# Optimization experiments

Measured on AMD Instinct MI355X. Metric: run time of the kernel, lower is better.

The kernel has to match this reference:

```python
import jax, jax.numpy as jnp
import numpy as np


def setup_inputs() -> dict:
    key = jax.random.key(0)
    k_u, k_a, k_b, k_c, k_d = jax.random.split(key, 5)
    B, T, Din, Dout, S = 16, 4096, 256, 256, 256
    return {
        "u": jax.random.normal(k_u, (B, T, Din), dtype=jnp.float32),
        "a_raw": jnp.zeros((S,), dtype=jnp.float32),
        "b": jax.random.normal(k_b, (S, Din), dtype=jnp.float32) * 0.1,
        "c": jax.random.normal(k_c, (Dout, S), dtype=jnp.float32) * 0.1,
        "d": jax.random.normal(k_d, (Dout, Din), dtype=jnp.float32) * 0.1,
    }


def reference(u, a_raw, b, c, d):
    # u: (B, T, Din) -> y: (B, T, Dout)
    # Recurrence: x_t = a * x_{t-1} + b @ u_t ;  y_t = c @ x_t + d @ u_t
    a = jnp.tanh(a_raw)                                  # (S,)
    Bu = jnp.einsum('btd,sd->bts', u, b)                 # input projection, (B,T,S)

    def step(x, bu_t):
        x = x * a + bu_t                                 # diagonal state update
        return x, x

    x0 = jnp.zeros((u.shape[0], a.shape[0]), dtype=u.dtype)
    _, xs = jax.lax.scan(step, x0, jnp.swapaxes(Bu, 0, 1))  # xs: (T,B,S)
    xs = jnp.swapaxes(xs, 0, 1)                              # (B,T,S)

    y = jnp.einsum('bts,os->bto', xs, c) + jnp.einsum('bti,oi->bto', u, d)
    return y  # dropout(p=0.0) is identity
```

## Files before the change

kernel.cpp:

```cpp
#include <hip/hip_runtime.h>

#define DEV __device__ __forceinline__

typedef unsigned short u16;
typedef __attribute__((ext_vector_type(8))) __bf16 bf16x8;
typedef __attribute__((ext_vector_type(4))) float f32x4;
typedef __attribute__((ext_vector_type(8))) unsigned short u16x8;

static constexpr int NB = 16;
static constexpr int NT = 4096;
static constexpr int ND = 256;
static constexpr int NM = NB * NT;
static constexpr int NCH = 64;
static constexpr int LCH = 64;

DEV u16 f2bf(float f) {
  unsigned u = __builtin_bit_cast(unsigned, f);
  u += 0x7fffu + ((u >> 16) & 1u);
  return (u16)(u >> 16);
}
DEV float bf2f(u16 h) {
  unsigned u = ((unsigned)h) << 16;
  return __builtin_bit_cast(float, u);
}

DEV void gl_lds16(const void* gp, void* lp) {
  __builtin_amdgcn_global_load_lds(
      (__attribute__((address_space(1))) void*)(void*)gp,
      (__attribute__((address_space(3))) void*)lp, 16, 0, 0);
}

__global__ __launch_bounds__(256) void prep_k(const float* __restrict__ a_raw,
                                              const float* __restrict__ b,
                                              const float* __restrict__ c,
                                              const float* __restrict__ d,
                                              float* __restrict__ af,
                                              u16* __restrict__ bw,
                                              u16* __restrict__ cw,
                                              u16* __restrict__ dw) {
  int i = blockIdx.x * 256 + threadIdx.x;
  if (i < 256) af[i] = tanhf(a_raw[i]);
  bw[i] = f2bf(b[i]);
  cw[i] = f2bf(c[i]);
  dw[i] = f2bf(d[i]);
}

__global__ __launch_bounds__(256) void convu_k(const float* __restrict__ u,
                                               u16* __restrict__ ub) {
  size_t i = ((size_t)blockIdx.x * 256 + threadIdx.x) * 8;
  float4 v0 = *reinterpret_cast<const float4*>(u + i);
  float4 v1 = *reinterpret_cast<const float4*>(u + i + 4);
  u16x8 o;
  o[0] = f2bf(v0.x); o[1] = f2bf(v0.y); o[2] = f2bf(v0.z); o[3] = f2bf(v0.w);
  o[4] = f2bf(v1.x); o[5] = f2bf(v1.y); o[6] = f2bf(v1.z); o[7] = f2bf(v1.w);
  *reinterpret_cast<u16x8*>(ub + i) = o;
}

template <int NSRC, bool OUT_BF16>
__global__ __launch_bounds__(256) void gemm_k(const u16* __restrict__ A0,
                                              const u16* __restrict__ B0,
                                              const u16* __restrict__ A1,
                                              const u16* __restrict__ B1,
                                              void* __restrict__ out) {
  __shared__ u16 As[128 * 64];
  __shared__ u16 Bs[128 * 64];
  const int tid = threadIdx.x;
  const int lane = tid & 63;
  const int wid = tid >> 6;
  const int wm = wid >> 1, wn = wid & 1;
  const int row0 = blockIdx.x * 128;
  const int col0 = blockIdx.y * 128;

  const int rstg = tid >> 3;
  const int c16 = tid & 7;

  const f32x4 zero = {0.f, 0.f, 0.f, 0.f};
  f32x4 acc[4][4];
#pragma unroll
  for (int i = 0; i < 4; ++i)
#pragma unroll
    for (int j = 0; j < 4; ++j) acc[i][j] = zero;

#pragma unroll
  for (int kt = 0; kt < 4 * NSRC; ++kt) {
    const u16* Ap = (NSRC == 2 && kt >= 4) ? A1 : A0;
    const u16* Bp = (NSRC == 2 && kt >= 4) ? B1 : B0;
    const int kb = (kt & 3) * 64;
#pragma unroll
    for (int j = 0; j < 4; ++j) {
      int row = j * 32 + rstg;
      int sc = c16 ^ (row & 7);
      gl_lds16(Ap + (size_t)(row0 + row) * 256 + kb + sc * 8,
               (char*)As + j * 4096 + wid * 1024);
      gl_lds16(Bp + (size_t)(col0 + row) * 256 + kb + sc * 8,
               (char*)Bs + j * 4096 + wid * 1024);
    }
    __syncthreads();
#pragma unroll
    for (int kk = 0; kk < 2; ++kk) {
      bf16x8 af[4], bfr[4];
#pragma unroll
      for (int mi = 0; mi < 4; ++mi) {
        int row = wm * 64 + mi * 16 + (lane & 15);
        int slot = (kk * 4 + (lane >> 4)) ^ (row & 7);
        af[mi] = *reinterpret_cast<const bf16x8*>(&As[row * 64 + slot * 8]);
      }
#pragma unroll
      for (int ni = 0; ni < 4; ++ni) {
        int row = wn * 64 + ni * 16 + (lane & 15);
        int slot = (kk * 4 + (lane >> 4)) ^ (row & 7);
        bfr[ni] = *reinterpret_cast<const bf16x8*>(&Bs[row * 64 + slot * 8]);
      }
#pragma unroll
      for (int mi = 0; mi < 4; ++mi)
#pragma unroll
        for (int ni = 0; ni < 4; ++ni)
          acc[mi][ni] = __builtin_amdgcn_mfma_f32_16x16x32_bf16(
              af[mi], bfr[ni], acc[mi][ni], 0, 0, 0);
    }
    __syncthreads();
  }

#pragma unroll
  for (int mi = 0; mi < 4; ++mi) {
    int rowb = row0 + wm * 64 + mi * 16 + (lane >> 4) * 4;
#pragma unroll
    for (int ni = 0; ni < 4; ++ni) {
      int colg = col0 + wn * 64 + ni * 16 + (lane & 15);
      f32x4 v = acc[mi][ni];
#pragma unroll
      for (int r = 0; r < 4; ++r) {
        size_t idx = (size_t)(rowb + r) * 256 + colg;
        if constexpr (OUT_BF16)
          ((u16*)out)[idx] = f2bf(v[r]);
        else
          ((float*)out)[idx] = v[r];
      }
    }
  }
}

__global__ __launch_bounds__(256) void scan1_k(const u16* __restrict__ bu,
                                               const float* __restrict__ af,
                                               float* __restrict__ carry) {
  int blk = blockIdx.x;
  int b = blk >> 6, ch = blk & 63;
  int s = threadIdx.x;
  float a = af[s];
  size_t base = ((size_t)(b * NT + ch * LCH)) * 256 + s;
  float x = 0.f;
  for (int tb = 0; tb < LCH; tb += 8) {
    float vb[8];
#pragma unroll
    for (int j = 0; j < 8; ++j) vb[j] = bf2f(bu[base + (size_t)(tb + j) * 256]);
#pragma unroll
    for (int j = 0; j < 8; ++j) x = fmaf(a, x, vb[j]);
  }
  carry[(size_t)blk * 256 + s] = x;
}

__global__ __launch_bounds__(256) void scan2_k(const float* __restrict__ carry,
                                               const float* __restrict__ af,
                                               float* __restrict__ initb) {
  int b = blockIdx.x;
  int s = threadIdx.x;
  float a = af[s];
  float aL = a;
#pragma unroll
  for (int i = 0; i < 6; ++i) aL *= aL;
  float x = 0.f;
  for (int k = 0; k < NCH; ++k) {
    size_t idx = ((size_t)(b * NCH + k)) * 256 + s;
    float cv = carry[idx];
    initb[idx] = x;
    x = fmaf(aL, x, cv);
  }
}

__global__ __launch_bounds__(256) void scan3_k(u16* __restrict__ bu,
                                               const float* __restrict__ af,
                                               const float* __restrict__ initb) {
  int blk = blockIdx.x;
  int b = blk >> 6, ch = blk & 63;
  int s = threadIdx.x;
  float a = af[s];
  float x = initb[(size_t)blk * 256 + s];
  size_t base = ((size_t)(b * NT + ch * LCH)) * 256 + s;
  for (int tb = 0; tb < LCH; tb += 8) {
    float vb[8];
#pragma unroll
    for (int j = 0; j < 8; ++j) vb[j] = bf2f(bu[base + (size_t)(tb + j) * 256]);
    u16 ob[8];
#pragma unroll
    for (int j = 0; j < 8; ++j) {
      x = fmaf(a, x, vb[j]);
      ob[j] = f2bf(x);
    }
#pragma unroll
    for (int j = 0; j < 8; ++j) bu[base + (size_t)(tb + j) * 256] = ob[j];
  }
}

extern "C" void kernel_launch(void* const* d_in, const int* in_sizes, int n_in,
                              void* d_out, int out_size, void* d_ws, size_t ws_size,
                              hipStream_t stream) {
  const float* u = (const float*)d_in[0];
  const float* a_raw = (const float*)d_in[1];
  const float* b = (const float*)d_in[2];
  const float* c = (const float*)d_in[3];
  const float* d = (const float*)d_in[4];
  float* y = (float*)d_out;
  char* ws = (char*)d_ws;

  float* af = (float*)(ws);
  u16* bw = (u16*)(ws + 4096);
  u16* cw = (u16*)(ws + 4096 + 131072);
  u16* dw = (u16*)(ws + 4096 + 2 * 131072);
  u16* ubf = (u16*)(ws + (1 << 20));
  u16* bu = (u16*)(ws + (1 << 20) + (size_t)32 * 1024 * 1024);
  float* carry = (float*)(ws + (1 << 20) + (size_t)64 * 1024 * 1024);
  float* initb = (float*)(ws + (2 << 20) + (size_t)64 * 1024 * 1024);

  prep_k<<<256, 256, 0, stream>>>(a_raw, b, c, d, af, bw, cw, dw);
  convu_k<<<8192, 256, 0, stream>>>(u, ubf);
  gemm_k<1, true><<<dim3(512, 2), 256, 0, stream>>>(ubf, bw, nullptr, nullptr, bu);
  scan1_k<<<1024, 256, 0, stream>>>(bu, af, carry);
  scan2_k<<<16, 256, 0, stream>>>(carry, af, initb);
  scan3_k<<<1024, 256, 0, stream>>>(bu, af, initb);
  gemm_k<2, false><<<dim3(512, 2), 256, 0, stream>>>(bu, cw, ubf, dw, y);
}
```

Measured before the change: 96.79 us.

## Fuse fp32 conversion into first GEMM and scan pass into second GEMM

Drops the separate u-to-bf16 conversion kernel by converting fp32 u inside the first GEMM. That GEMM now also computes the D·u product, which the second GEMM uses as its accumulator initial value. The third scan pass moves into the second GEMM: each block loads a 128-row bu tile into LDS, runs the chunk recurrence in place, then multiplies by C. It also stores bu in a swizzled layout so it can be bulk-copied to LDS, and widens the scan1 loads. This removes several full-tensor round trips through HBM. The cost is a larger LDS footprint (about 80KB per block), which limits occupancy, plus a serial 64-step scan inside the GEMM before the MFMA work starts.

```diff
diff --git a/kernel.cpp b/kernel.cpp
--- a/kernel.cpp
+++ b/kernel.cpp
@@ -6,11 +6,10 @@
 typedef __attribute__((ext_vector_type(8))) __bf16 bf16x8;
 typedef __attribute__((ext_vector_type(4))) float f32x4;
 typedef __attribute__((ext_vector_type(8))) unsigned short u16x8;
+typedef __attribute__((ext_vector_type(4))) unsigned short u16x4;
 
 static constexpr int NB = 16;
 static constexpr int NT = 4096;
-static constexpr int ND = 256;
-static constexpr int NM = NB * NT;
 static constexpr int NCH = 64;
 static constexpr int LCH = 64;
 
@@ -28,6 +27,13 @@
   __builtin_amdgcn_global_load_lds(
       (__attribute__((address_space(1))) void*)(void*)gp,
       (__attribute__((address_space(3))) void*)lp, 16, 0, 0);
+}
+
+DEV u16x8 pack8(float4 a, float4 b) {
+  u16x8 o;
+  o[0] = f2bf(a.x); o[1] = f2bf(a.y); o[2] = f2bf(a.z); o[3] = f2bf(a.w);
+  o[4] = f2bf(b.x); o[5] = f2bf(b.y); o[6] = f2bf(b.z); o[7] = f2bf(b.w);
+  return o;
 }
 
 __global__ __launch_bounds__(256) void prep_k(const float* __restrict__ a_raw,
@@ -45,96 +51,89 @@
   dw[i] = f2bf(d[i]);
 }
 
-__global__ __launch_bounds__(256) void convu_k(const float* __restrict__ u,
-                                               u16* __restrict__ ub) {
-  size_t i = ((size_t)blockIdx.x * 256 + threadIdx.x) * 8;
-  float4 v0 = *reinterpret_cast<const float4*>(u + i);
-  float4 v1 = *reinterpret_cast<const float4*>(u + i + 4);
-  u16x8 o;
-  o[0] = f2bf(v0.x); o[1] = f2bf(v0.y); o[2] = f2bf(v0.z); o[3] = f2bf(v0.w);
-  o[4] = f2bf(v1.x); o[5] = f2bf(v1.y); o[6] = f2bf(v1.z); o[7] = f2bf(v1.w);
-  *reinterpret_cast<u16x8*>(ub + i) = o;
-}
-
-template <int NSRC, bool OUT_BF16>
-__global__ __launch_bounds__(256) void gemm_k(const u16* __restrict__ A0,
-                                              const u16* __restrict__ B0,
-                                              const u16* __restrict__ A1,
-                                              const u16* __restrict__ B1,
-                                              void* __restrict__ out) {
+__global__ __launch_bounds__(512) void gemm1_k(const float* __restrict__ u,
+                                               const u16* __restrict__ bw,
+                                               const u16* __restrict__ dw,
+                                               u16* __restrict__ bu,
+                                               u16* __restrict__ ud) {
   __shared__ u16 As[128 * 64];
   __shared__ u16 Bs[128 * 64];
   const int tid = threadIdx.x;
   const int lane = tid & 63;
   const int wid = tid >> 6;
-  const int wm = wid >> 1, wn = wid & 1;
-  const int row0 = blockIdx.x * 128;
-  const int col0 = blockIdx.y * 128;
-
-  const int rstg = tid >> 3;
-  const int c16 = tid & 7;
+  const int wr = wid >> 2, wc = wid & 3;
+  const int bx = blockIdx.x;
+  const int by = blockIdx.y;
+  const bool dpanel = (by >= 2);
+  const int col0 = (by & 1) * 128;
+  const u16* W = dpanel ? dw : bw;
+  const size_t row0 = (size_t)bx * 128;
+
+  const int arow = tid >> 2;
+  const int ak0 = (tid & 3) * 16;
+  const float* uptr = u + (row0 + arow) * 256;
+  const int s0 = (tid & 3) * 2;
 
   const f32x4 zero = {0.f, 0.f, 0.f, 0.f};
-  f32x4 acc[4][4];
-#pragma unroll
-  for (int i = 0; i < 4; ++i)
-#pragma unroll
-    for (int j = 0; j < 4; ++j) acc[i][j] = zero;
-
-#pragma unroll
-  for (int kt = 0; kt < 4 * NSRC; ++kt) {
-    const u16* Ap = (NSRC == 2 && kt >= 4) ? A1 : A0;
-    const u16* Bp = (NSRC == 2 && kt >= 4) ? B1 : B0;
-    const int kb = (kt & 3) * 64;
-#pragma unroll
-    for (int j = 0; j < 4; ++j) {
-      int row = j * 32 + rstg;
-      int sc = c16 ^ (row & 7);
-      gl_lds16(Ap + (size_t)(row0 + row) * 256 + kb + sc * 8,
-               (char*)As + j * 4096 + wid * 1024);
-      gl_lds16(Bp + (size_t)(col0 + row) * 256 + kb + sc * 8,
-               (char*)Bs + j * 4096 + wid * 1024);
-    }
+  f32x4 acc[4][2];
+#pragma unroll
+  for (int i = 0; i < 4; ++i) { acc[i][0] = zero; acc[i][1] = zero; }
+
+#pragma unroll
+  for (int kt = 0; kt < 4; ++kt) {
+    const int kb = kt * 64;
+    float4 f0 = *reinterpret_cast<const float4*>(uptr + kb + ak0);
+    float4 f1 = *reinterpret_cast<const float4*>(uptr + kb + ak0 + 4);
+    float4 f2 = *reinterpret_cast<const float4*>(uptr + kb + ak0 + 8);
+    float4 f3 = *reinterpret_cast<const float4*>(uptr + kb + ak0 + 12);
+#pragma unroll
+    for (int r = 0; r < 2; ++r) {
+      int brow = r * 64 + (tid >> 3);
+      int sc = (tid & 7) ^ (brow & 7);
+      gl_lds16(W + (size_t)(col0 + brow) * 256 + kb + sc * 8,
+               (char*)Bs + r * 8192 + wid * 1024);
+    }
+    *reinterpret_cast<u16x8*>(&As[arow * 64 + ((s0) ^ (arow & 7)) * 8]) = pack8(f0, f1);
+    *reinterpret_cast<u16x8*>(&As[arow * 64 + ((s0 + 1) ^ (arow & 7)) * 8]) = pack8(f2, f3);
     __syncthreads();
 #pragma unroll
     for (int kk = 0; kk < 2; ++kk) {
-      bf16x8 af[4], bfr[4];
+      const int ks = kk * 4 + (lane >> 4);
+      bf16x8 afr[4], bfr[2];
 #pragma unroll
       for (int mi = 0; mi < 4; ++mi) {
-        int row = wm * 64 + mi * 16 + (lane & 15);
-        int slot = (kk * 4 + (lane >> 4)) ^ (row & 7);
-        af[mi] = *reinterpret_cast<const bf16x8*>(&As[row * 64 + slot * 8]);
-      }
-#pragma unroll
-      for (int ni = 0; ni < 4; ++ni) {
-        int row = wn * 64 + ni * 16 + (lane & 15);
-        int slot = (kk * 4 + (lane >> 4)) ^ (row & 7);
-        bfr[ni] = *reinterpret_cast<const bf16x8*>(&Bs[row * 64 + slot * 8]);
+        int ar = wr * 64 + mi * 16 + (lane & 15);
+        afr[mi] = *reinterpret_cast<const bf16x8*>(&As[ar * 64 + (ks ^ (ar & 7)) * 8]);
+      }
+#pragma unroll
+      for (int ni = 0; ni < 2; ++ni) {
+        int nr = wc * 32 + ni * 16 + (lane & 15);
+        bfr[ni] = *reinterpret_cast<const bf16x8*>(&Bs[nr * 64 + (ks ^ (nr & 7)) * 8]);
       }
 #pragma unroll
       for (int mi = 0; mi < 4; ++mi)
 #pragma unroll
-        for (int ni = 0; ni < 4; ++ni)
+        for (int ni = 0; ni < 2; ++ni)
           acc[mi][ni] = __builtin_amdgcn_mfma_f32_16x16x32_bf16(
-              af[mi], bfr[ni], acc[mi][ni], 0, 0, 0);
-    }
-    __syncthreads();
+              afr[mi], bfr[ni], acc[mi][ni], 0, 0, 0);
+    }
+    if (kt < 3) __syncthreads();
   }
 
 #pragma unroll
   for (int mi = 0; mi < 4; ++mi) {
-    int rowb = row0 + wm * 64 + mi * 16 + (lane >> 4) * 4;
-#pragma unroll
-    for (int ni = 0; ni < 4; ++ni) {
-      int colg = col0 + wn * 64 + ni * 16 + (lane & 15);
-      f32x4 v = acc[mi][ni];
-#pragma unroll
-      for (int r = 0; r < 4; ++r) {
-        size_t idx = (size_t)(rowb + r) * 256 + colg;
-        if constexpr (OUT_BF16)
-          ((u16*)out)[idx] = f2bf(v[r]);
+    int rlb = wr * 64 + mi * 16 + (lane >> 4) * 4;
+#pragma unroll
+    for (int ni = 0; ni < 2; ++ni) {
+      int col = col0 + wc * 32 + ni * 16 + (lane & 15);
+#pragma unroll
+      for (int q = 0; q < 4; ++q) {
+        size_t R = row0 + rlb + q;
+        u16 h = f2bf(acc[mi][ni][q]);
+        if (!dpanel)
+          bu[R * 256 + (((col >> 3) ^ ((int)(R) & 7)) * 8) + (col & 7)] = h;
         else
-          ((float*)out)[idx] = v[r];
+          ud[R * 256 + col] = h;
       }
     }
   }
@@ -143,20 +142,22 @@
 __global__ __launch_bounds__(256) void scan1_k(const u16* __restrict__ bu,
                                                const float* __restrict__ af,
                                                float* __restrict__ carry) {
-  int blk = blockIdx.x;
-  int b = blk >> 6, ch = blk & 63;
-  int s = threadIdx.x;
-  float a = af[s];
-  size_t base = ((size_t)(b * NT + ch * LCH)) * 256 + s;
-  float x = 0.f;
-  for (int tb = 0; tb < LCH; tb += 8) {
-    float vb[8];
-#pragma unroll
-    for (int j = 0; j < 8; ++j) vb[j] = bf2f(bu[base + (size_t)(tb + j) * 256]);
-#pragma unroll
-    for (int j = 0; j < 8; ++j) x = fmaf(a, x, vb[j]);
-  }
-  carry[(size_t)blk * 256 + s] = x;
+  const int tid = threadIdx.x;
+  const int g = blockIdx.x * 4 + (tid >> 6);
+  const int s4 = (tid & 63) * 4;
+  const size_t rb = (size_t)g * 64;
+  float a0 = af[s4], a1 = af[s4 + 1], a2 = af[s4 + 2], a3 = af[s4 + 3];
+  float x0 = 0.f, x1 = 0.f, x2 = 0.f, x3 = 0.f;
+  for (int t = 0; t < LCH; ++t) {
+    size_t idx = (rb + t) * 256 + ((s4 >> 3) ^ (t & 7)) * 8 + (s4 & 7);
+    u16x4 v = *reinterpret_cast<const u16x4*>(bu + idx);
+    x0 = fmaf(a0, x0, bf2f(v[0]));
+    x1 = fmaf(a1, x1, bf2f(v[1]));
+    x2 = fmaf(a2, x2, bf2f(v[2]));
+    x3 = fmaf(a3, x3, bf2f(v[3]));
+  }
+  float4 o = {x0, x1, x2, x3};
+  *reinterpret_cast<float4*>(carry + (size_t)g * 256 + s4) = o;
 }
 
 __global__ __launch_bounds__(256) void scan2_k(const float* __restrict__ carry,
@@ -177,27 +178,112 @@
   }
 }
 
-__global__ __launch_bounds__(256) void scan3_k(u16* __restrict__ bu,
+__global__ __launch_bounds__(512) void gemm2_k(const u16* __restrict__ bu,
+                                               const u16* __restrict__ cw,
+                                               const u16* __restrict__ ud,
                                                const float* __restrict__ af,
-                                               const float* __restrict__ initb) {
-  int blk = blockIdx.x;
-  int b = blk >> 6, ch = blk & 63;
-  int s = threadIdx.x;
-  float a = af[s];
-  float x = initb[(size_t)blk * 256 + s];
-  size_t base = ((size_t)(b * NT + ch * LCH)) * 256 + s;
-  for (int tb = 0; tb < LCH; tb += 8) {
-    float vb[8];
-#pragma unroll
-    for (int j = 0; j < 8; ++j) vb[j] = bf2f(bu[base + (size_t)(tb + j) * 256]);
-    u16 ob[8];
-#pragma unroll
-    for (int j = 0; j < 8; ++j) {
-      x = fmaf(a, x, vb[j]);
-      ob[j] = f2bf(x);
-    }
-#pragma unroll
-    for (int j = 0; j < 8; ++j) bu[base + (size_t)(tb + j) * 256] = ob[j];
+                                               const float* __restrict__ initb,
+                                               float* __restrict__ y) {
+  __shared__ u16 XS[128 * 256];
+  __shared__ u16 CS[128 * 64];
+  const int tid = threadIdx.x;
+  const int lane = tid & 63;
+  const int wid = tid >> 6;
+  const int wr = wid >> 2, wc = wid & 3;
+  const int bx = blockIdx.x;
+  const int col0 = blockIdx.y * 128;
+
+  const char* src = (const char*)bu + (size_t)bx * 65536;
+#pragma unroll
+  for (int j = 0; j < 8; ++j)
+    gl_lds16(src + j * 8192 + tid * 16, (char*)XS + j * 8192 + wid * 1024);
+#pragma unroll
+  for (int r = 0; r < 2; ++r) {
+    int brow = r * 64 + (tid >> 3);
+    int sc = (tid & 7) ^ (brow & 7);
+    gl_lds16(cw + (size_t)(col0 + brow) * 256 + 0 + sc * 8,
+             (char*)CS + r * 8192 + wid * 1024);
+  }
+  __syncthreads();
+
+  {
+    const int hf = tid >> 8;
+    const int s = tid & 255;
+    const float a = af[s];
+    float x = initb[(size_t)(bx * 2 + hf) * 256 + s];
+    const int r0 = hf * 64;
+    const int slot = s >> 3;
+    const int off = (s & 7);
+#pragma unroll 8
+    for (int t = 0; t < 64; ++t) {
+      int r = r0 + t;
+      int bi = r * 256 + ((slot ^ (r & 7)) * 8) + off;
+      x = fmaf(a, x, bf2f(XS[bi]));
+      XS[bi] = f2bf(x);
+    }
+  }
+
+  f32x4 acc[4][2];
+#pragma unroll
+  for (int mi = 0; mi < 4; ++mi) {
+    int rlb = wr * 64 + mi * 16 + (lane >> 4) * 4;
+#pragma unroll
+    for (int ni = 0; ni < 2; ++ni) {
+      int col = col0 + wc * 32 + ni * 16 + (lane & 15);
+#pragma unroll
+      for (int q = 0; q < 4; ++q)
+        acc[mi][ni][q] = bf2f(ud[(size_t)(bx * 128 + rlb + q) * 256 + col]);
+    }
+  }
+  __syncthreads();
+
+#pragma unroll
+  for (int kt = 0; kt < 4; ++kt) {
+#pragma unroll
+    for (int kk = 0; kk < 2; ++kk) {
+      const int ksl = kk * 4 + (lane >> 4);
+      const int ksg = kt * 8 + ksl;
+      bf16x8 afr[4], bfr[2];
+#pragma unroll
+      for (int mi = 0; mi < 4; ++mi) {
+        int ar = wr * 64 + mi * 16 + (lane & 15);
+        afr[mi] = *reinterpret_cast<const bf16x8*>(&XS[ar * 256 + ((ksg ^ (ar & 7)) * 8)]);
+      }
+#pragma unroll
+      for (int ni = 0; ni < 2; ++ni) {
+        int nr = wc * 32 + ni * 16 + (lane & 15);
+        bfr[ni] = *reinterpret_cast<const bf16x8*>(&CS[nr * 64 + ((ksl ^ (nr & 7)) * 8)]);
+      }
+#pragma unroll
+      for (int mi = 0; mi < 4; ++mi)
+#pragma unroll
+        for (int ni = 0; ni < 2; ++ni)
+          acc[mi][ni] = __builtin_amdgcn_mfma_f32_16x16x32_bf16(
+              afr[mi], bfr[ni], acc[mi][ni], 0, 0, 0);
+    }
+    if (kt < 3) {
+      __syncthreads();
+#pragma unroll
+      for (int r = 0; r < 2; ++r) {
+        int brow = r * 64 + (tid >> 3);
+        int sc = (tid & 7) ^ (brow & 7);
+        gl_lds16(cw + (size_t)(col0 + brow) * 256 + (kt + 1) * 64 + sc * 8,
+                 (char*)CS + r * 8192 + wid * 1024);
+      }
+      __syncthreads();
+    }
+  }
+
+#pragma unroll
+  for (int mi = 0; mi < 4; ++mi) {
+    int rlb = wr * 64 + mi * 16 + (lane >> 4) * 4;
+#pragma unroll
+    for (int ni = 0; ni < 2; ++ni) {
+      int col = col0 + wc * 32 + ni * 16 + (lane & 15);
+#pragma unroll
+      for (int q = 0; q < 4; ++q)
+        y[(size_t)(bx * 128 + rlb + q) * 256 + col] = acc[mi][ni][q];
+    }
   }
 }
 
@@ -212,20 +298,19 @@
   float* y = (float*)d_out;
   char* ws = (char*)d_ws;
 
+  const size_t MB = 1u << 20;
   float* af = (float*)(ws);
   u16* bw = (u16*)(ws + 4096);
   u16* cw = (u16*)(ws + 4096 + 131072);
   u16* dw = (u16*)(ws + 4096 + 2 * 131072);
-  u16* ubf = (u16*)(ws + (1 << 20));
-  u16* bu = (u16*)(ws + (1 << 20) + (size_t)32 * 1024 * 1024);
-  float* carry = (float*)(ws + (1 << 20) + (size_t)64 * 1024 * 1024);
-  float* initb = (float*)(ws + (2 << 20) + (size_t)64 * 1024 * 1024);
+  u16* bu = (u16*)(ws + 1 * MB);
+  u16* ud = (u16*)(ws + 33 * MB);
+  float* carry = (float*)(ws + 65 * MB);
+  float* initb = (float*)(ws + 66 * MB);
 
   prep_k<<<256, 256, 0, stream>>>(a_raw, b, c, d, af, bw, cw, dw);
-  convu_k<<<8192, 256, 0, stream>>>(u, ubf);
-  gemm_k<1, true><<<dim3(512, 2), 256, 0, stream>>>(ubf, bw, nullptr, nullptr, bu);
-  scan1_k<<<1024, 256, 0, stream>>>(bu, af, carry);
+  gemm1_k<<<dim3(512, 4), 512, 0, stream>>>(u, bw, dw, bu, ud);
+  scan1_k<<<256, 256, 0, stream>>>(bu, af, carry);
   scan2_k<<<16, 256, 0, stream>>>(carry, af, initb);
-  scan3_k<<<1024, 256, 0, stream>>>(bu, af, initb);
-  gemm_k<2, false><<<dim3(512, 2), 256, 0, stream>>>(bu, cw, ubf, dw, y);
-}
+  gemm2_k<<<dim3(512, 2), 512, 0, stream>>>(bu, cw, ud, af, initb, y);
+}
```

Measured after the change: 107.3 us. 1.11x slower.
